# Optimization experiments

Hardware: AMD Instinct MI355X
Metric: run time of the kernel (lower is better)

## Reference

```python
import jax, jax.numpy as jnp
import numpy as np

D_MODEL = 1024
N_HEADS = 16
D_HEAD = D_MODEL // N_HEADS
D_FF = 4096
B, T = 2, 2048


def setup_inputs() -> dict:
    key = jax.random.key(0)
    ks = jax.random.split(key, 7)
    s = lambda fan_in: 1.0 / np.sqrt(fan_in)
    return {
        "x": jax.random.normal(ks[0], (B, T, D_MODEL), dtype=jnp.float32),
        "ln1_g": jnp.ones((D_MODEL,), jnp.float32),
        "ln1_b": jnp.zeros((D_MODEL,), jnp.float32),
        "w_qkv": jax.random.normal(ks[1], (D_MODEL, 3 * D_MODEL), jnp.float32) * s(D_MODEL),
        "w_proj": jax.random.normal(ks[2], (D_MODEL, D_MODEL), jnp.float32) * s(D_MODEL),
        "ln2_g": jnp.ones((D_MODEL,), jnp.float32),
        "ln2_b": jnp.zeros((D_MODEL,), jnp.float32),
        "w_fc1": jax.random.normal(ks[3], (D_MODEL, D_FF), jnp.float32) * s(D_MODEL),
        "w_fc2": jax.random.normal(ks[4], (D_FF, D_MODEL), jnp.float32) * s(D_FF),
    }


def _layernorm(x, g, b, eps=1e-5):
    mu = jnp.mean(x, axis=-1, keepdims=True)
    var = jnp.var(x, axis=-1, keepdims=True)
    return (x - mu) * jax.lax.rsqrt(var + eps) * g + b


def _attn(x, w_qkv, w_proj):
    Bx, Tx, d = x.shape
    qkv = x @ w_qkv  # [B,T,3d]
    q, k, v = jnp.split(qkv, 3, axis=-1)
    split = lambda t: t.reshape(Bx, Tx, N_HEADS, D_HEAD).transpose(0, 2, 1, 3)
    q, k, v = split(q), split(k), split(v)
    scores = jnp.einsum("bhqd,bhkd->bhqk", q, k) / np.sqrt(D_HEAD).astype(np.float32)
    mask = jnp.tril(jnp.ones((Tx, Tx), dtype=bool))
    scores = jnp.where(mask, scores, -jnp.inf)
    attn = jax.nn.softmax(scores, axis=-1)
    out = jnp.einsum("bhqk,bhkd->bhqd", attn, v)
    out = out.transpose(0, 2, 1, 3).reshape(Bx, Tx, d)
    return out @ w_proj


def reference(x, ln1_g, ln1_b, w_qkv, w_proj, ln2_g, ln2_b, w_fc1, w_fc2):
    x = x + _attn(_layernorm(x, ln1_g, ln1_b), w_qkv, w_proj)
    h = jax.nn.gelu(_layernorm(x, ln2_g, ln2_b) @ w_fc1, approximate=False)
    return x + h @ w_fc2
```

## Files before the change

### kernel.cpp

```cpp
#include <hip/hip_runtime.h>
#include <math.h>

using short8 = __attribute__((ext_vector_type(8))) short;
using f32x4  = __attribute__((ext_vector_type(4))) float;
typedef unsigned short ushort;

__device__ inline ushort f2bf(float f) {
    union { float f; unsigned int i; } v; v.f = f;
    unsigned int x = v.i;
    return (ushort)((x + 0x7FFFu + ((x >> 16) & 1u)) >> 16);
}
__device__ inline void st_out(float* p, float v) { *p = v; }
__device__ inline void st_out(ushort* p, float v) { *p = f2bf(v); }

__device__ inline void gl_lds16(const ushort* g, ushort* l) {
    __builtin_amdgcn_global_load_lds((const __attribute__((address_space(1))) unsigned int*)g,
                                     (__attribute__((address_space(3))) unsigned int*)l, 16, 0, 0);
}
#define MFMA __builtin_amdgcn_mfma_f32_16x16x32_bf16

__global__ __launch_bounds__(256) void ln_kernel(const float* __restrict__ x,
                                                 const float* __restrict__ g,
                                                 const float* __restrict__ b,
                                                 ushort* __restrict__ y) {
    int row = blockIdx.x;
    const float* xr = x + (size_t)row * 1024;
    int t = threadIdx.x;
    float v[4];
    float s = 0.f, s2 = 0.f;
#pragma unroll
    for (int i = 0; i < 4; i++) {
        v[i] = xr[t + i * 256];
        s += v[i]; s2 += v[i] * v[i];
    }
#pragma unroll
    for (int off = 1; off < 64; off <<= 1) {
        s += __shfl_xor(s, off); s2 += __shfl_xor(s2, off);
    }
    __shared__ float ps[8];
    int w = t >> 6;
    if ((t & 63) == 0) { ps[w] = s; ps[4 + w] = s2; }
    __syncthreads();
    s  = ps[0] + ps[1] + ps[2] + ps[3];
    s2 = ps[4] + ps[5] + ps[6] + ps[7];
    float mu   = s * (1.0f / 1024.0f);
    float var  = s2 * (1.0f / 1024.0f) - mu * mu;
    float rinv = rsqrtf(var + 1e-5f);
    ushort* yr = y + (size_t)row * 1024;
#pragma unroll
    for (int i = 0; i < 4; i++) {
        int c = t + i * 256;
        yr[c] = f2bf((v[i] - mu) * rinv * g[c] + b[c]);
    }
}

__global__ __launch_bounds__(256) void wt_kernel(const float* __restrict__ s,
                                                 ushort* __restrict__ d, int K, int N) {
    __shared__ float tile[32][33];
    int n0 = blockIdx.x * 32, k0 = blockIdx.y * 32;
    int tx = threadIdx.x & 31, ty = threadIdx.x >> 5;
#pragma unroll
    for (int i = 0; i < 4; i++)
        tile[ty + i * 8][tx] = s[(size_t)(k0 + ty + i * 8) * N + n0 + tx];
    __syncthreads();
#pragma unroll
    for (int i = 0; i < 4; i++)
        d[(size_t)(n0 + ty + i * 8) * K + k0 + tx] = f2bf(tile[tx][ty + i * 8]);
}

template <int EPI, typename CT>
__global__ __launch_bounds__(256) void gemm_kernel(const ushort* __restrict__ A,
                                                   const ushort* __restrict__ Bt,
                                                   CT* __restrict__ C,
                                                   const float* __restrict__ R,
                                                   ushort* __restrict__ VT,
                                                   int M, int N, int K) {
    __shared__ alignas(16) ushort As[128 * 64];
    __shared__ alignas(16) ushort Bs[128 * 64];
    int t = threadIdx.x, lane = t & 63, w = t >> 6;
    int bm = blockIdx.y * 128, bn = blockIdx.x * 128;
    int wm = (w >> 1) * 64, wn = (w & 1) * 64;
    f32x4 acc[4][4] = {};
    int srow = lane >> 3;
    int schunk = (lane & 7) ^ (lane >> 3);
    int rs = lane & 15, qd = lane >> 4;

    for (int k0 = 0; k0 < K; k0 += 64) {
        __syncthreads();
#pragma unroll
        for (int i = 0; i < 4; i++) {
            int rr = w * 32 + i * 8;
            gl_lds16(A  + (size_t)(bm + rr + srow) * K + k0 + schunk * 8, &As[rr * 64]);
            gl_lds16(Bt + (size_t)(bn + rr + srow) * K + k0 + schunk * 8, &Bs[rr * 64]);
        }
        __syncthreads();
#pragma unroll
        for (int half = 0; half < 2; half++) {
            int cq = qd + half * 4;
            short8 af[4], bf[4];
#pragma unroll
            for (int i = 0; i < 4; i++) {
                int ml = wm + i * 16 + rs;
                af[i] = *(const short8*)&As[ml * 64 + ((cq ^ (ml & 7)) * 8)];
                int nl = wn + i * 16 + rs;
                bf[i] = *(const short8*)&Bs[nl * 64 + ((cq ^ (nl & 7)) * 8)];
            }
#pragma unroll
            for (int mi = 0; mi < 4; mi++)
#pragma unroll
                for (int ni = 0; ni < 4; ni++)
                    acc[mi][ni] = MFMA(af[mi], bf[ni], acc[mi][ni], 0, 0, 0);
        }
    }
#pragma unroll
    for (int mi = 0; mi < 4; mi++)
#pragma unroll
        for (int ni = 0; ni < 4; ni++) {
            int row = bm + wm + mi * 16 + qd * 4;
            int col = bn + wn + ni * 16 + rs;
            if (EPI == 3) {
                if (col < 2048) {
#pragma unroll
                    for (int r = 0; r < 4; r++)
                        ((ushort*)C)[(size_t)(row + r) * 2048 + col] = f2bf(acc[mi][ni][r]);
                } else {
                    int rel = col - 2048, hh = rel >> 6, dd = rel & 63;
                    ushort tmp[4];
#pragma unroll
                    for (int r = 0; r < 4; r++) tmp[r] = f2bf(acc[mi][ni][r]);
                    size_t base = ((size_t)((row >> 11) * 16 + hh) * 64 + dd) * 2048 + (row & 2047);
                    *(uint2*)&VT[base] = *(uint2*)tmp;
                }
            } else {
#pragma unroll
                for (int r = 0; r < 4; r++) {
                    float v = acc[mi][ni][r];
                    size_t idx = (size_t)(row + r) * N + col;
                    if (EPI == 1) v += R[idx];
                    if (EPI == 2) v = 0.5f * v * (1.0f + erff(v * 0.70710678118f));
                    st_out(&C[idx], v);
                }
            }
        }
}

template <int EPI, typename CT>
__global__ __launch_bounds__(256) void gemm_n64_kernel(const ushort* __restrict__ A,
                                                       const ushort* __restrict__ Bt,
                                                       CT* __restrict__ C,
                                                       const float* __restrict__ R,
                                                       int M, int N, int K, int Kh) {
    __shared__ alignas(16) ushort As[128 * 64];
    __shared__ alignas(16) ushort Bs[64 * 64];
    int t = threadIdx.x, lane = t & 63, w = t >> 6;
    int bm = blockIdx.x * 128, bn = blockIdx.y * 64;
    int kbeg = blockIdx.z * Kh;
    int wm = (w >> 1) * 64, wn = (w & 1) * 32;
    f32x4 acc[4][2] = {};
    int srow = lane >> 3;
    int schunk = (lane & 7) ^ (lane >> 3);
    int rs = lane & 15, qd = lane >> 4;

    for (int k0 = kbeg; k0 < kbeg + Kh; k0 += 64) {
        __syncthreads();
#pragma unroll
        for (int i = 0; i < 4; i++) {
            int rr = w * 32 + i * 8;
            gl_lds16(A + (size_t)(bm + rr + srow) * K + k0 + schunk * 8, &As[rr * 64]);
        }
#pragma unroll
        for (int i = 0; i < 2; i++) {
            int rr = w * 16 + i * 8;
            gl_lds16(Bt + (size_t)(bn + rr + srow) * K + k0 + schunk * 8, &Bs[rr * 64]);
        }
        __syncthreads();
#pragma unroll
        for (int half = 0; half < 2; half++) {
            int cq = qd + half * 4;
            short8 af[4], bfr[2];
#pragma unroll
            for (int i = 0; i < 4; i++) {
                int ml = wm + i * 16 + rs;
                af[i] = *(const short8*)&As[ml * 64 + ((cq ^ (ml & 7)) * 8)];
            }
#pragma unroll
            for (int j = 0; j < 2; j++) {
                int nl = wn + j * 16 + rs;
                bfr[j] = *(const short8*)&Bs[nl * 64 + ((cq ^ (nl & 7)) * 8)];
            }
#pragma unroll
            for (int mi = 0; mi < 4; mi++)
#pragma unroll
                for (int ni = 0; ni < 2; ni++)
                    acc[mi][ni] = MFMA(af[mi], bfr[ni], acc[mi][ni], 0, 0, 0);
        }
    }
#pragma unroll
    for (int mi = 0; mi < 4; mi++)
#pragma unroll
        for (int ni = 0; ni < 2; ni++) {
            int row = bm + wm + mi * 16 + qd * 4;
            int col = bn + wn + ni * 16 + rs;
#pragma unroll
            for (int r = 0; r < 4; r++) {
                float v = acc[mi][ni][r];
                size_t idx = (size_t)(row + r) * N + col;
                if (EPI == 4) {
                    atomicAdd((float*)&C[idx], v);
                } else {
                    if (EPI == 1) v += R[idx];
                    st_out(&C[idx], v);
                }
            }
        }
}

__global__ __launch_bounds__(256) void attn_kernel(const ushort* __restrict__ qk,
                                                   const ushort* __restrict__ vT,
                                                   float* __restrict__ accO,
                                                   float* __restrict__ accL) {
    int qi = blockIdx.x;
    int nk = qi / 2 + 1;
    int t0 = blockIdx.z * 4;
    if (t0 >= nk) return;
    int t1 = min(t0 + 4, nk);
    __shared__ alignas(16) ushort Ks[128 * 64];
    __shared__ alignas(16) ushort VTs[64 * 128];
    __shared__ alignas(16) ushort Ps[4 * 16 * 136];
    int t = threadIdx.x, lane = t & 63, w = t >> 6;
    int q0 = qi * 64;
    int bh = blockIdx.y, bb = bh >> 4, h = bh & 15;
    const ushort* qkb = qk + (size_t)bb * 2048 * 2048;
    const ushort* qptr = qkb + h * 64;
    const ushort* kptr = qkb + 1024 + h * 64;
    const ushort* vtb  = vT + (size_t)bh * 64 * 2048;
    int rs = lane & 15, qd = lane >> 4;
    int qrow = q0 + w * 16 + rs;
    short8 aq0 = *(const short8*)(qptr + (size_t)qrow * 2048 + qd * 8);
    short8 aq1 = *(const short8*)(qptr + (size_t)qrow * 2048 + 32 + qd * 8);
    f32x4 o_acc[4] = {};
    float l_part[4] = {0.f, 0.f, 0.f, 0.f};
    int myq = q0 + w * 16 + qd * 4;
    int krl = lane >> 3, kch = lane & 7;
    int vrl = lane >> 4, vch = lane & 15;

    for (int kt = t0; kt < t1; kt++) {
        int k0 = kt * 128;
        __syncthreads();
#pragma unroll
        for (int i = 0; i < 4; i++) {
            int kk = w * 32 + i * 8 + krl;
            gl_lds16(kptr + (size_t)(k0 + kk) * 2048 + ((kch ^ (kk & 7)) * 8), &Ks[(w * 32 + i * 8) * 64]);
            int dd = w * 16 + i * 4 + vrl;
            gl_lds16(vtb + (size_t)dd * 2048 + k0 + ((vch ^ (dd & 15)) * 8), &VTs[(w * 16 + i * 4) * 128]);
        }
        __syncthreads();
        f32x4 s[8];
#pragma unroll
        for (int c = 0; c < 8; c++) {
            int kk = c * 16 + rs;
            short8 kf0 = *(const short8*)&Ks[kk * 64 + ((qd ^ (kk & 7)) * 8)];
            short8 kf1 = *(const short8*)&Ks[kk * 64 + (((qd + 4) ^ (kk & 7)) * 8)];
            f32x4 z = {};
            z = MFMA(aq0, kf0, z, 0, 0, 0);
            z = MFMA(aq1, kf1, z, 0, 0, 0);
            s[c] = z;
        }
        bool lastt = (kt == nk - 1);
#pragma unroll
        for (int c = 0; c < 8; c++) {
            int kk = k0 + c * 16 + rs;
#pragma unroll
            for (int r = 0; r < 4; r++) {
                float p = __expf(s[c][r] * 0.125f);
                if (lastt && (kk > myq + r)) p = 0.f;
                s[c][r] = p;
                l_part[r] += p;
            }
        }
#pragma unroll
        for (int r = 0; r < 4; r++)
#pragma unroll
            for (int c = 0; c < 8; c++)
                Ps[(w * 16 + qd * 4 + r) * 136 + c * 16 + rs] = f2bf(s[c][r]);
        short8 ap[4];
#pragma unroll
        for (int kc = 0; kc < 4; kc++)
            ap[kc] = *(const short8*)&Ps[(w * 16 + rs) * 136 + kc * 32 + qd * 8];
#pragma unroll
        for (int dt = 0; dt < 4; dt++) {
            int dd = dt * 16 + rs;
#pragma unroll
            for (int kc = 0; kc < 4; kc++) {
                int g = kc * 4 + qd;
                short8 bv = *(const short8*)&VTs[dd * 128 + ((g ^ (dd & 15)) * 8)];
                o_acc[dt] = MFMA(ap[kc], bv, o_acc[dt], 0, 0, 0);
            }
        }
    }
#pragma unroll
    for (int r = 0; r < 4; r++)
#pragma unroll
        for (int off = 1; off < 16; off <<= 1)
            l_part[r] += __shfl_xor(l_part[r], off);
#pragma unroll
    for (int dt = 0; dt < 4; dt++)
#pragma unroll
        for (int r = 0; r < 4; r++)
            atomicAdd(&accO[(size_t)(bb * 2048 + myq + r) * 1024 + h * 64 + dt * 16 + rs], o_acc[dt][r]);
    if (rs == 0)
#pragma unroll
        for (int r = 0; r < 4; r++)
            atomicAdd(&accL[(size_t)(bb * 2048 + myq + r) * 16 + h], l_part[r]);
}

__global__ __launch_bounds__(256) void attn_fin_kernel(const float* __restrict__ accO,
                                                       const float* __restrict__ accL,
                                                       ushort* __restrict__ outp) {
    int row = blockIdx.x;
    int c0 = threadIdx.x * 4;
    float inv = 1.0f / accL[row * 16 + (c0 >> 6)];
    float4 o = *(const float4*)(accO + (size_t)row * 1024 + c0);
    ushort r4[4] = { f2bf(o.x * inv), f2bf(o.y * inv), f2bf(o.z * inv), f2bf(o.w * inv) };
    *(uint2*)(outp + (size_t)row * 1024 + c0) = *(uint2*)r4;
}

extern "C" void kernel_launch(void* const* d_in, const int* in_sizes, int n_in,
                              void* d_out, int out_size, void* d_ws, size_t ws_size,
                              hipStream_t stream) {
    const float* x     = (const float*)d_in[0];
    const float* ln1g  = (const float*)d_in[1];
    const float* ln1b  = (const float*)d_in[2];
    const float* wqkv  = (const float*)d_in[3];
    const float* wproj = (const float*)d_in[4];
    const float* ln2g  = (const float*)d_in[5];
    const float* ln2b  = (const float*)d_in[6];
    const float* wfc1  = (const float*)d_in[7];
    const float* wfc2  = (const float*)d_in[8];
    float* out = (float*)d_out;
    char* ws = (char*)d_ws;
    const size_t MB = 1024 * 1024;

    ushort* wbufA = (ushort*)(ws);
    ushort* lnbuf = (ushort*)(ws + 8 * MB);
    ushort* qk    = (ushort*)(ws + 16 * MB);
    ushort* vT    = (ushort*)(ws + 32 * MB);
    float*  accL  = (float*)(ws + 40 * MB);
    float*  accO  = out;
    const int Rr = 4096;

    ln_kernel<<<Rr, 256, 0, stream>>>(x, ln1g, ln1b, lnbuf);
    wt_kernel<<<dim3(3072 / 32, 1024 / 32), 256, 0, stream>>>(wqkv, wbufA, 1024, 3072);
    gemm_kernel<3, ushort><<<dim3(3072 / 128, Rr / 128), 256, 0, stream>>>(lnbuf, wbufA, qk, nullptr, vT, Rr, 3072, 1024);
    hipMemsetAsync(accO, 0, (size_t)Rr * 1024 * 4, stream);
    hipMemsetAsync(accL, 0, (size_t)Rr * 16 * 4, stream);
    attn_kernel<<<dim3(32, 32, 4), 256, 0, stream>>>(qk, vT, accO, accL);
    attn_fin_kernel<<<Rr, 256, 0, stream>>>(accO, accL, lnbuf);
    wt_kernel<<<dim3(1024 / 32, 1024 / 32), 256, 0, stream>>>(wproj, wbufA, 1024, 1024);
    gemm_n64_kernel<1, float><<<dim3(Rr / 128, 1024 / 64, 1), 256, 0, stream>>>(lnbuf, wbufA, out, x, Rr, 1024, 1024, 1024);
    ln_kernel<<<Rr, 256, 0, stream>>>(out, ln2g, ln2b, lnbuf);
    wt_kernel<<<dim3(4096 / 32, 1024 / 32), 256, 0, stream>>>(wfc1, wbufA, 1024, 4096);

    if (ws_size >= 56 * MB) {
        ushort* hmid  = qk;
        ushort* wbufB = (ushort*)(ws + 48 * MB);
        wt_kernel<<<dim3(1024 / 32, 4096 / 32), 256, 0, stream>>>(wfc2, wbufB, 4096, 1024);
        gemm_kernel<2, ushort><<<dim3(4096 / 128, Rr / 128), 256, 0, stream>>>(lnbuf, wbufA, hmid, nullptr, nullptr, Rr, 4096, 1024);
        gemm_n64_kernel<4, float><<<dim3(Rr / 128, 1024 / 64, 2), 256, 0, stream>>>(hmid, wbufB, out, nullptr, Rr, 1024, 4096, 2048);
    } else {
        ushort* hmid  = qk;
        ushort* wbufB = (ushort*)(ws + 32 * MB);
        wt_kernel<<<dim3(1024 / 32, 4096 / 32), 256, 0, stream>>>(wfc2, wbufB, 4096, 1024);
        for (int hf = 0; hf < 2; hf++) {
            const ushort* lnh = lnbuf + (size_t)hf * 2048 * 1024;
            float* outh = out + (size_t)hf * 2048 * 1024;
            gemm_kernel<2, ushort><<<dim3(4096 / 128, 2048 / 128), 256, 0, stream>>>(lnh, wbufA, hmid, nullptr, nullptr, 2048, 4096, 1024);
            gemm_n64_kernel<4, float><<<dim3(2048 / 128, 1024 / 64, 2), 256, 0, stream>>>(hmid, wbufB, outh, nullptr, 2048, 1024, 4096, 2048);
        }
    }
}
```

Baseline: 404.8 us.

## Pair causal query tiles for balanced attention split and drop atomics/memsets

```diff
diff --git a/kernel.cpp b/kernel.cpp
--- a/kernel.cpp
+++ b/kernel.cpp
@@ -9,6 +9,10 @@
     union { float f; unsigned int i; } v; v.f = f;
     unsigned int x = v.i;
     return (ushort)((x + 0x7FFFu + ((x >> 16) & 1u)) >> 16);
+}
+__device__ inline ushort f2bf_hu(float f) {
+    union { float f; unsigned int i; } v; v.f = f;
+    return (ushort)((v.i + 0x8000u) >> 16);
 }
 __device__ inline void st_out(float* p, float v) { *p = v; }
 __device__ inline void st_out(ushort* p, float v) { *p = f2bf(v); }
@@ -120,9 +124,10 @@
             int col = bn + wn + ni * 16 + rs;
             if (EPI == 3) {
                 if (col < 2048) {
+                    float sc = (col < 1024) ? 0.125f : 1.0f;
 #pragma unroll
                     for (int r = 0; r < 4; r++)
-                        ((ushort*)C)[(size_t)(row + r) * 2048 + col] = f2bf(acc[mi][ni][r]);
+                        ((ushort*)C)[(size_t)(row + r) * 2048 + col] = f2bf(acc[mi][ni][r] * sc);
                 } else {
                     int rel = col - 2048, hh = rel >> 6, dd = rel & 63;
                     ushort tmp[4];
@@ -217,112 +222,140 @@
 
 __global__ __launch_bounds__(256) void attn_kernel(const ushort* __restrict__ qk,
                                                    const ushort* __restrict__ vT,
-                                                   float* __restrict__ accO,
-                                                   float* __restrict__ accL) {
-    int qi = blockIdx.x;
-    int nk = qi / 2 + 1;
-    int t0 = blockIdx.z * 4;
-    if (t0 >= nk) return;
-    int t1 = min(t0 + 4, nk);
+                                                   ushort* __restrict__ attnO,
+                                                   float* __restrict__ pO,
+                                                   float* __restrict__ pL) {
     __shared__ alignas(16) ushort Ks[128 * 64];
     __shared__ alignas(16) ushort VTs[64 * 128];
-    __shared__ alignas(16) ushort Ps[4 * 16 * 136];
     int t = threadIdx.x, lane = t & 63, w = t >> 6;
-    int q0 = qi * 64;
-    int bh = blockIdx.y, bb = bh >> 4, h = bh & 15;
+    int p = blockIdx.x, bh = blockIdx.y, z = blockIdx.z;
+    int bb = bh >> 4, h = bh & 15;
     const ushort* qkb = qk + (size_t)bb * 2048 * 2048;
     const ushort* qptr = qkb + h * 64;
     const ushort* kptr = qkb + 1024 + h * 64;
     const ushort* vtb  = vT + (size_t)bh * 64 * 2048;
     int rs = lane & 15, qd = lane >> 4;
-    int qrow = q0 + w * 16 + rs;
-    short8 aq0 = *(const short8*)(qptr + (size_t)qrow * 2048 + qd * 8);
-    short8 aq1 = *(const short8*)(qptr + (size_t)qrow * 2048 + 32 + qd * 8);
-    f32x4 o_acc[4] = {};
-    float l_part[4] = {0.f, 0.f, 0.f, 0.f};
-    int myq = q0 + w * 16 + qd * 4;
     int krl = lane >> 3, kch = lane & 7;
     int vrl = lane >> 4, vch = lane & 15;
-
-    for (int kt = t0; kt < t1; kt++) {
-        int k0 = kt * 128;
-        __syncthreads();
-#pragma unroll
-        for (int i = 0; i < 4; i++) {
-            int kk = w * 32 + i * 8 + krl;
-            gl_lds16(kptr + (size_t)(k0 + kk) * 2048 + ((kch ^ (kk & 7)) * 8), &Ks[(w * 32 + i * 8) * 64]);
-            int dd = w * 16 + i * 4 + vrl;
-            gl_lds16(vtb + (size_t)dd * 2048 + k0 + ((vch ^ (dd & 15)) * 8), &VTs[(w * 16 + i * 4) * 128]);
-        }
-        __syncthreads();
-        f32x4 s[8];
-#pragma unroll
-        for (int c = 0; c < 8; c++) {
-            int kk = c * 16 + rs;
-            short8 kf0 = *(const short8*)&Ks[kk * 64 + ((qd ^ (kk & 7)) * 8)];
-            short8 kf1 = *(const short8*)&Ks[kk * 64 + (((qd + 4) ^ (kk & 7)) * 8)];
-            f32x4 z = {};
-            z = MFMA(aq0, kf0, z, 0, 0, 0);
-            z = MFMA(aq1, kf1, z, 0, 0, 0);
-            s[c] = z;
-        }
-        bool lastt = (kt == nk - 1);
-#pragma unroll
-        for (int c = 0; c < 8; c++) {
-            int kk = k0 + c * 16 + rs;
+    int nkA = p / 2 + 1, nkB = (31 - p) / 2 + 1;
+    int qts[2] = {p, 31 - p};
+    int nks[2] = {nkA, nkB};
+    int kb[2], ke[2];
+    if (z == 0) { kb[0] = 0; ke[0] = nkA; kb[1] = 0;       ke[1] = 9 - nkA; }
+    else        { kb[0] = 0; ke[0] = 0;   kb[1] = 9 - nkA; ke[1] = nkB;     }
+    ushort* Pw = &Ks[w * 2048];
+
+    for (int ph = 0; ph < 2; ph++) {
+        if (kb[ph] >= ke[ph]) continue;
+        int qt = qts[ph], nk = nks[ph];
+        int q0 = qt * 64;
+        int qrow = q0 + w * 16 + rs;
+        short8 aq0 = *(const short8*)(qptr + (size_t)qrow * 2048 + qd * 8);
+        short8 aq1 = *(const short8*)(qptr + (size_t)qrow * 2048 + 32 + qd * 8);
+        int myq = q0 + w * 16 + qd * 4;
+        f32x4 o_acc[4] = {};
+        float l_part[4] = {0.f, 0.f, 0.f, 0.f};
+
+        for (int kt = kb[ph]; kt < ke[ph]; kt++) {
+            int k0 = kt * 128;
+            __syncthreads();
+#pragma unroll
+            for (int i = 0; i < 4; i++) {
+                int kk = w * 32 + i * 8 + krl;
+                gl_lds16(kptr + (size_t)(k0 + kk) * 2048 + ((kch ^ (kk & 7)) * 8), &Ks[(w * 32 + i * 8) * 64]);
+                int dd = w * 16 + i * 4 + vrl;
+                gl_lds16(vtb + (size_t)dd * 2048 + k0 + ((vch ^ (dd & 15)) * 8), &VTs[(w * 16 + i * 4) * 128]);
+            }
+            __syncthreads();
+            f32x4 s[8];
+#pragma unroll
+            for (int c = 0; c < 8; c++) {
+                int kk = c * 16 + rs;
+                short8 kf0 = *(const short8*)&Ks[kk * 64 + ((qd ^ (kk & 7)) * 8)];
+                short8 kf1 = *(const short8*)&Ks[kk * 64 + (((qd + 4) ^ (kk & 7)) * 8)];
+                f32x4 zz = {};
+                zz = MFMA(aq0, kf0, zz, 0, 0, 0);
+                zz = MFMA(aq1, kf1, zz, 0, 0, 0);
+                s[c] = zz;
+            }
+            bool lastt = (kt == nk - 1);
+#pragma unroll
+            for (int c = 0; c < 8; c++) {
+                int kk = k0 + c * 16 + rs;
+#pragma unroll
+                for (int r = 0; r < 4; r++) {
+                    float pv = __expf(s[c][r]);
+                    if (lastt && (kk > myq + r)) pv = 0.f;
+                    s[c][r] = pv;
+                    l_part[r] += pv;
+                }
+            }
+            __syncthreads();
 #pragma unroll
             for (int r = 0; r < 4; r++) {
-                float p = __expf(s[c][r] * 0.125f);
-                if (lastt && (kk > myq + r)) p = 0.f;
-                s[c][r] = p;
-                l_part[r] += p;
+                int row = qd * 4 + r;
+#pragma unroll
+                for (int c = 0; c < 8; c++) {
+                    int chunk = c * 2 + (rs >> 3);
+                    Pw[row * 128 + ((chunk ^ row) * 8) + (rs & 7)] = f2bf_hu(s[c][r]);
+                }
+            }
+            short8 ap[4];
+#pragma unroll
+            for (int kc = 0; kc < 4; kc++)
+                ap[kc] = *(const short8*)&Pw[rs * 128 + (((kc * 4 + qd) ^ rs) * 8)];
+#pragma unroll
+            for (int dt = 0; dt < 4; dt++) {
+                int dd = dt * 16 + rs;
+#pragma unroll
+                for (int kc = 0; kc < 4; kc++) {
+                    int g = kc * 4 + qd;
+                    short8 bv = *(const short8*)&VTs[dd * 128 + ((g ^ (dd & 15)) * 8)];
+                    o_acc[dt] = MFMA(ap[kc], bv, o_acc[dt], 0, 0, 0);
+                }
             }
         }
 #pragma unroll
         for (int r = 0; r < 4; r++)
 #pragma unroll
-            for (int c = 0; c < 8; c++)
-                Ps[(w * 16 + qd * 4 + r) * 136 + c * 16 + rs] = f2bf(s[c][r]);
-        short8 ap[4];
-#pragma unroll
-        for (int kc = 0; kc < 4; kc++)
-            ap[kc] = *(const short8*)&Ps[(w * 16 + rs) * 136 + kc * 32 + qd * 8];
-#pragma unroll
-        for (int dt = 0; dt < 4; dt++) {
-            int dd = dt * 16 + rs;
-#pragma unroll
-            for (int kc = 0; kc < 4; kc++) {
-                int g = kc * 4 + qd;
-                short8 bv = *(const short8*)&VTs[dd * 128 + ((g ^ (dd & 15)) * 8)];
-                o_acc[dt] = MFMA(ap[kc], bv, o_acc[dt], 0, 0, 0);
-            }
-        }
-    }
-#pragma unroll
-    for (int r = 0; r < 4; r++)
-#pragma unroll
-        for (int off = 1; off < 16; off <<= 1)
-            l_part[r] += __shfl_xor(l_part[r], off);
-#pragma unroll
-    for (int dt = 0; dt < 4; dt++)
-#pragma unroll
-        for (int r = 0; r < 4; r++)
-            atomicAdd(&accO[(size_t)(bb * 2048 + myq + r) * 1024 + h * 64 + dt * 16 + rs], o_acc[dt][r]);
-    if (rs == 0)
-#pragma unroll
-        for (int r = 0; r < 4; r++)
-            atomicAdd(&accL[(size_t)(bb * 2048 + myq + r) * 16 + h], l_part[r]);
-}
-
-__global__ __launch_bounds__(256) void attn_fin_kernel(const float* __restrict__ accO,
-                                                       const float* __restrict__ accL,
-                                                       ushort* __restrict__ outp) {
-    int row = blockIdx.x;
-    int c0 = threadIdx.x * 4;
-    float inv = 1.0f / accL[row * 16 + (c0 >> 6)];
-    float4 o = *(const float4*)(accO + (size_t)row * 1024 + c0);
-    ushort r4[4] = { f2bf(o.x * inv), f2bf(o.y * inv), f2bf(o.z * inv), f2bf(o.w * inv) };
-    *(uint2*)(outp + (size_t)row * 1024 + c0) = *(uint2*)r4;
+            for (int off = 1; off < 16; off <<= 1)
+                l_part[r] += __shfl_xor(l_part[r], off);
+        if (ph == 0) {
+#pragma unroll
+            for (int dt = 0; dt < 4; dt++)
+#pragma unroll
+                for (int r = 0; r < 4; r++)
+                    attnO[(size_t)(bb * 2048 + myq + r) * 1024 + h * 64 + dt * 16 + rs] =
+                        f2bf(o_acc[dt][r] / l_part[r]);
+        } else {
+            int qb16 = 15 - p;
+            size_t ob = ((size_t)(z * 32 + bh) * 16 + qb16) * 4096;
+#pragma unroll
+            for (int dt = 0; dt < 4; dt++)
+#pragma unroll
+                for (int r = 0; r < 4; r++)
+                    pO[ob + (size_t)(w * 16 + qd * 4 + r) * 64 + dt * 16 + rs] = o_acc[dt][r];
+            if (rs == 0)
+#pragma unroll
+                for (int r = 0; r < 4; r++)
+                    pL[((size_t)(z * 32 + bh) * 16 + qb16) * 64 + w * 16 + qd * 4 + r] = l_part[r];
+        }
+    }
+}
+
+__global__ __launch_bounds__(256) void attn_comb_kernel(const float* __restrict__ pO,
+                                                        const float* __restrict__ pL,
+                                                        ushort* __restrict__ attnO) {
+    int idx4 = (blockIdx.x * 256 + threadIdx.x) * 4;
+    int dim = idx4 & 63, row = (idx4 >> 6) & 63, qb = (idx4 >> 12) & 15, bh = idx4 >> 16;
+    float4 o0 = *(const float4*)(pO + idx4);
+    float4 o1 = *(const float4*)(pO + 2097152 + idx4);
+    float inv = 1.0f / (pL[idx4 >> 6] + pL[32768 + (idx4 >> 6)]);
+    int grow = (bh >> 4) * 2048 + (16 + qb) * 64 + row;
+    int col = (bh & 15) * 64 + dim;
+    ushort r4[4] = { f2bf((o0.x + o1.x) * inv), f2bf((o0.y + o1.y) * inv),
+                     f2bf((o0.z + o1.z) * inv), f2bf((o0.w + o1.w) * inv) };
+    *(uint2*)(attnO + (size_t)grow * 1024 + col) = *(uint2*)r4;
 }
 
 extern "C" void kernel_launch(void* const* d_in, const int* in_sizes, int n_in,
@@ -345,17 +378,14 @@
     ushort* lnbuf = (ushort*)(ws + 8 * MB);
     ushort* qk    = (ushort*)(ws + 16 * MB);
     ushort* vT    = (ushort*)(ws + 32 * MB);
-    float*  accL  = (float*)(ws + 40 * MB);
-    float*  accO  = out;
+    float*  pL    = (float*)(ws + 40 * MB);
     const int Rr = 4096;
 
     ln_kernel<<<Rr, 256, 0, stream>>>(x, ln1g, ln1b, lnbuf);
     wt_kernel<<<dim3(3072 / 32, 1024 / 32), 256, 0, stream>>>(wqkv, wbufA, 1024, 3072);
     gemm_kernel<3, ushort><<<dim3(3072 / 128, Rr / 128), 256, 0, stream>>>(lnbuf, wbufA, qk, nullptr, vT, Rr, 3072, 1024);
-    hipMemsetAsync(accO, 0, (size_t)Rr * 1024 * 4, stream);
-    hipMemsetAsync(accL, 0, (size_t)Rr * 16 * 4, stream);
-    attn_kernel<<<dim3(32, 32, 4), 256, 0, stream>>>(qk, vT, accO, accL);
-    attn_fin_kernel<<<Rr, 256, 0, stream>>>(accO, accL, lnbuf);
+    attn_kernel<<<dim3(16, 32, 2), 256, 0, stream>>>(qk, vT, lnbuf, out, pL);
+    attn_comb_kernel<<<2048, 256, 0, stream>>>(out, pL, lnbuf);
     wt_kernel<<<dim3(1024 / 32, 1024 / 32), 256, 0, stream>>>(wproj, wbufA, 1024, 1024);
     gemm_n64_kernel<1, float><<<dim3(Rr / 128, 1024 / 64, 1), 256, 0, stream>>>(lnbuf, wbufA, out, x, Rr, 1024, 1024, 1024);
     ln_kernel<<<Rr, 256, 0, stream>>>(out, ln2g, ln2b, lnbuf);
```

Result: faster. 368.9 us (-8.9%).
